# Optimization experiments

Measured on AMD Instinct MI355X. Metric: run time of the kernel, lower is better.

The kernel has to match this reference:

```python
import jax, jax.numpy as jnp
import numpy as np

K = 20
EPS = 1e-5


def knn_idx(x, k=K):
    # x: [B, C, N]; negative squared pairwise distance, take k largest (nearest)
    xt = jnp.swapaxes(x, 1, 2)  # [B, N, C]
    inner = -2.0 * jnp.einsum('bnc,bmc->bnm', xt, xt)
    xx = jnp.sum(x * x, axis=1)  # [B, N]
    dist = -xx[:, :, None] - inner - xx[:, None, :]  # [B, N, N] = -||xi-xj||^2
    _, idx = jax.lax.top_k(dist, k)  # [B, N, k]
    return idx


def edge_features(x, k=K):
    # returns [B, 2C, N, k] = concat(neighbor - center, center)
    idx = knn_idx(x, k)
    xt = jnp.swapaxes(x, 1, 2)  # [B, N, C]
    neigh = jax.vmap(lambda xb, ib: xb[ib])(xt, idx)  # [B, N, k, C]
    center = jnp.broadcast_to(xt[:, :, None, :], neigh.shape)
    feat = jnp.concatenate((neigh - center, center), axis=-1)  # [B, N, k, 2C]
    return jnp.transpose(feat, (0, 3, 1, 2))  # [B, 2C, N, k]


def bn_relu(y, g, b, axes):
    # batch-norm (training-mode batch stats, biased var) + ReLU; channel axis=1
    mu = jnp.mean(y, axis=axes, keepdims=True)
    var = jnp.mean(jnp.square(y - mu), axis=axes, keepdims=True)
    shape = [1] * y.ndim
    shape[1] = -1
    yhat = (y - mu) * jax.lax.rsqrt(var + EPS)
    return jax.nn.relu(yhat * g.reshape(shape) + b.reshape(shape))


def attn_pool(y):
    # softmax over neighbor axis, weighted sum: [B, C, N, k] -> [B, C, N]
    a = jax.nn.softmax(y, axis=-1)
    return jnp.sum(y * a, axis=-1)


def reference(x, W1, g1, b1, W2, g2, b2, W3, g3, b3):
    feat = edge_features(x)  # [B, 6, N, k]
    h1 = bn_relu(jnp.einsum('oc,bcnk->bonk', W1, feat), g1, b1, (0, 2, 3))  # [B,64,N,k]
    x1 = attn_pool(h1)  # [B, 64, N]
    h2 = bn_relu(jnp.einsum('oc,bcnk->bonk', W2, h1), g2, b2, (0, 2, 3))  # [B,128,N,k]
    x2 = attn_pool(h2)  # [B, 128, N]
    cat = jnp.concatenate((x1, x2), axis=1)  # [B, 192, N]
    out = bn_relu(jnp.einsum('oc,bcn->bon', W3, cat), g3, b3, (0, 2))  # [B,256,N]
    return out


def setup_inputs() -> dict:
    key = jax.random.key(0)
    ks = jax.random.split(key, 4)
    B, C, N = 8, 3, 4096
    return {
        'x': jax.random.normal(ks[0], (B, C, N), jnp.float32),
        'W1': jax.random.normal(ks[1], (64, 6), jnp.float32) * 0.1,
        'g1': jnp.ones((64,), jnp.float32),
        'b1': jnp.zeros((64,), jnp.float32),
        'W2': jax.random.normal(ks[2], (128, 64), jnp.float32) * 0.1,
        'g2': jnp.ones((128,), jnp.float32),
        'b2': jnp.zeros((128,), jnp.float32),
        'W3': jax.random.normal(ks[3], (256, 192), jnp.float32) * 0.1,
        'g3': jnp.ones((256,), jnp.float32),
        'b3': jnp.zeros((256,), jnp.float32),
    }
```

## Files before the change

kernel.cpp:

```cpp
#include <hip/hip_runtime.h>

namespace {
constexpr int Bn  = 8;
constexpr int Nn  = 4096;
constexpr int KKn = 20;
constexpr int C1n = 64;
constexpr int C2n = 128;
constexpr int C3n = 256;
constexpr float EPSc = 1e-5f;
constexpr float INV_CNT1 = 1.0f / (8.0f * 4096.0f * 20.0f);
constexpr float INV_CNT3 = 1.0f / (8.0f * 4096.0f);
constexpr float INFK = 3.0e38f;
constexpr size_t IDX_N = (size_t)Bn * Nn * KKn;
constexpr int NBLK_KNN = (Bn * Nn) / 16;
}

#define DEVI __device__ __forceinline__

__global__ void k_zero(float* __restrict__ p) {
    const int i = blockIdx.x * 256 + threadIdx.x;
    if (i < 33664) p[i] = 0.0f;
}

DEVI void ins3(float d, int j, float& m0, float& m1, float& m2,
               int& j0, int& j1, int& j2) {
    if (d < m2) {
        if (d < m1) {
            m2 = m1; j2 = j1;
            if (d < m0) { m1 = m0; j1 = j0; m0 = d; j0 = j; }
            else        { m1 = d;  j1 = j; }
        } else { m2 = d; j2 = j; }
    }
}

__global__ __launch_bounds__(256) void k_knn(const float* __restrict__ x,
                                             int* __restrict__ idxout,
                                             float* __restrict__ Pbuf) {
    __shared__ int   lidx[16][KKn];
    __shared__ float red[4][27];
    const int b = blockIdx.y;
    const float* xb = x + (size_t)b * 3 * Nn;
    const int lane = threadIdx.x & 63;
    const int wave = threadIdx.x >> 6;
    const int rowbase = blockIdx.x * 16 + wave * 4;

    for (int su = 0; su < 2; ++su) {
        const int rA = rowbase + su * 2;
        const int rB = rA + 1;
        const float pxA = xb[rA], pyA = xb[Nn + rA], pzA = xb[2 * Nn + rA];
        const float pxB = xb[rB], pyB = xb[Nn + rB], pzB = xb[2 * Nn + rB];
        float mA0 = INFK, mA1 = INFK, mA2 = INFK;
        float mB0 = INFK, mB1 = INFK, mB2 = INFK;
        int jA0 = -1, jA1 = -1, jA2 = -1;
        int jB0 = -1, jB1 = -1, jB2 = -1;
        #pragma unroll 8
        for (int t = 0; t < 64; ++t) {
            const int j = t * 64 + lane;
            const float xj = xb[j], yj = xb[Nn + j], zj = xb[2 * Nn + j];
            const float dxA = pxA - xj, dyA = pyA - yj, dzA = pzA - zj;
            const float dA = fmaf(dxA, dxA, fmaf(dyA, dyA, dzA * dzA));
            const float dxB = pxB - xj, dyB = pyB - yj, dzB = pzB - zj;
            const float dB = fmaf(dxB, dxB, fmaf(dyB, dyB, dzB * dzB));
            ins3(dA, j, mA0, mA1, mA2, jA0, jA1, jA2);
            ins3(dB, j, mB0, mB1, mB2, jB0, jB1, jB2);
        }
        int nvA = 3, nvB = 3;
        for (int s = 0; s < KKn; ++s) {
            float bdA = (nvA > 0) ? mA0 : INFK;
            int   bjA = (nvA > 0) ? jA0 : -1;
            float bdB = (nvB > 0) ? mB0 : INFK;
            int   bjB = (nvB > 0) ? jB0 : -1;
            #pragma unroll
            for (int off = 32; off; off >>= 1) {
                const float odA = __shfl_xor(bdA, off);
                const int   ojA = __shfl_xor(bjA, off);
                const float odB = __shfl_xor(bdB, off);
                const int   ojB = __shfl_xor(bjB, off);
                if (odA < bdA || (odA == bdA && (unsigned)ojA < (unsigned)bjA)) { bdA = odA; bjA = ojA; }
                if (odB < bdB || (odB == bdB && (unsigned)ojB < (unsigned)bjB)) { bdB = odB; bjB = ojB; }
            }
            if (lane == 0) {
                lidx[wave * 4 + su * 2][s]     = bjA;
                lidx[wave * 4 + su * 2 + 1][s] = bjB;
            }
            if (nvA > 0 && jA0 == bjA) {
                mA0 = mA1; jA0 = jA1; mA1 = mA2; jA1 = jA2; --nvA;
                if (nvA == 0 && s < KKn - 1) {
                    mA0 = mA1 = mA2 = INFK; jA0 = jA1 = jA2 = -1;
                    #pragma unroll 1
                    for (int t = 0; t < 64; ++t) {
                        const int j = t * 64 + lane;
                        const float dx = pxA - xb[j], dy = pyA - xb[Nn + j], dz = pzA - xb[2 * Nn + j];
                        const float d = fmaf(dx, dx, fmaf(dy, dy, dz * dz));
                        if ((d > bdA) || (d == bdA && j > bjA))
                            ins3(d, j, mA0, mA1, mA2, jA0, jA1, jA2);
                    }
                    nvA = 3;
                }
            }
            if (nvB > 0 && jB0 == bjB) {
                mB0 = mB1; jB0 = jB1; mB1 = mB2; jB1 = jB2; --nvB;
                if (nvB == 0 && s < KKn - 1) {
                    mB0 = mB1 = mB2 = INFK; jB0 = jB1 = jB2 = -1;
                    #pragma unroll 1
                    for (int t = 0; t < 64; ++t) {
                        const int j = t * 64 + lane;
                        const float dx = pxB - xb[j], dy = pyB - xb[Nn + j], dz = pzB - xb[2 * Nn + j];
                        const float d = fmaf(dx, dx, fmaf(dy, dy, dz * dz));
                        if ((d > bdB) || (d == bdB && j > bjB))
                            ins3(d, j, mB0, mB1, mB2, jB0, jB1, jB2);
                    }
                    nvB = 3;
                }
            }
        }
    }
    __syncthreads();

    float S[6] = {};
    float M[21] = {};
    #pragma unroll
    for (int rep = 0; rep < 2; ++rep) {
        const int w = rep * 64 + lane;
        if (w < 4 * KKn) {
            const int r  = (w * 3277) >> 16;
            const int kk = w - r * 20;
            const int rowg = rowbase + r;
            const int j = lidx[wave * 4 + r][kk];
            const float cx = xb[rowg], cy = xb[Nn + rowg], cz = xb[2 * Nn + rowg];
            const float e[6] = { xb[j] - cx, xb[Nn + j] - cy, xb[2 * Nn + j] - cz, cx, cy, cz };
            int q = 0;
            #pragma unroll
            for (int a = 0; a < 6; ++a) {
                S[a] += e[a];
                #pragma unroll
                for (int bb = a; bb < 6; ++bb) { M[q] = fmaf(e[a], e[bb], M[q]); ++q; }
            }
            idxout[(size_t)(b * Nn + rowbase) * KKn + w] = j;
        }
    }
    #pragma unroll
    for (int i = 0; i < 6; ++i) {
        float t = S[i];
        #pragma unroll
        for (int off = 1; off < 64; off <<= 1) t += __shfl_xor(t, off);
        S[i] = t;
    }
    #pragma unroll
    for (int i = 0; i < 21; ++i) {
        float t = M[i];
        #pragma unroll
        for (int off = 1; off < 64; off <<= 1) t += __shfl_xor(t, off);
        M[i] = t;
    }
    if (lane == 0) {
        #pragma unroll
        for (int i = 0; i < 6; ++i) red[wave][i] = S[i];
        #pragma unroll
        for (int i = 0; i < 21; ++i) red[wave][6 + i] = M[i];
    }
    __syncthreads();
    if (threadIdx.x < 27) {
        const int i = threadIdx.x;
        const int blk = blockIdx.y * gridDim.x + blockIdx.x;
        Pbuf[blk * 32 + i] = red[0][i] + red[1][i] + red[2][i] + red[3][i];
    }
}

__global__ __launch_bounds__(256) void k_statK(const float* __restrict__ Pbuf,
                                               float* __restrict__ statK) {
    __shared__ float red[8][27];
    const int tid = threadIdx.x;
    const int i  = tid & 31;
    const int c0 = tid >> 5;
    if (i < 27) {
        float s = 0.f;
        for (int c = c0; c < NBLK_KNN; c += 8) s += Pbuf[c * 32 + i];
        red[c0][i] = s;
    }
    __syncthreads();
    if (tid < 27) {
        float s = 0.f;
        #pragma unroll
        for (int c = 0; c < 8; ++c) s += red[c][tid];
        statK[tid] = s;
    }
}

DEVI void bn1_coef(const float* __restrict__ statK, const float* __restrict__ W1,
                   const float* __restrict__ g1, const float* __restrict__ b1,
                   int o, float& a1, float& be1, float* w1r) {
    #pragma unroll
    for (int c = 0; c < 6; ++c) w1r[c] = W1[o * 6 + c];
    float s1 = 0.f, q1 = 0.f;
    #pragma unroll
    for (int a = 0; a < 6; ++a) s1 = fmaf(w1r[a], statK[a], s1);
    int qi = 6;
    #pragma unroll
    for (int a = 0; a < 6; ++a) {
        #pragma unroll
        for (int bb = a; bb < 6; ++bb) {
            const float coef = (a == bb ? 1.f : 2.f) * w1r[a] * w1r[bb];
            q1 = fmaf(coef, statK[qi], q1); ++qi;
        }
    }
    const float mu  = s1 * INV_CNT1;
    const float var = q1 * INV_CNT1 - mu * mu;
    const float rs  = rsqrtf(var + EPSc);
    a1  = rs * g1[o];
    be1 = fmaf(-mu, a1, b1[o]);
}

template <bool POOL>
DEVI void conv1_phase1(const float* __restrict__ x, const int* __restrict__ idx,
                       float a1, float be1, const float* w1r,
                       float* __restrict__ cat, int b, int n0, int tid,
                       float (*hhat)[64], float* sAcc) {
    const int o = tid & 63;
    const int wave = tid >> 6;
    const float* xb = x + (size_t)b * 3 * Nn;
    #pragma unroll
    for (int pp = 0; pp < 2; ++pp) {
        const int p = wave * 2 + pp;
        const int n = n0 + p;
        const float cx = xb[n], cy = xb[Nn + n], cz = xb[2 * Nn + n];
        const float t2 = fmaf(w1r[3], cx, fmaf(w1r[4], cy, w1r[5] * cz));
        float hk[KKn];
        #pragma unroll
        for (int kk = 0; kk < KKn; ++kk) {
            const int j = idx[(size_t)(b * Nn + n) * KKn + kk];
            const float dx = xb[j] - cx, dy = xb[Nn + j] - cy, dz = xb[2 * Nn + j] - cz;
            float h = fmaf(w1r[0], dx, fmaf(w1r[1], dy, fmaf(w1r[2], dz, t2)));
            h = fmaxf(fmaf(h, a1, be1), 0.0f);
            hk[kk] = h;
            hhat[p * KKn + kk][o] = h;
            if (POOL) *sAcc += h;
        }
        if (POOL) {
            float mx = hk[0];
            #pragma unroll
            for (int kk = 1; kk < KKn; ++kk) mx = fmaxf(mx, hk[kk]);
            float se = 0.0f, sw = 0.0f;
            #pragma unroll
            for (int kk = 0; kk < KKn; ++kk) {
                const float e = __expf(hk[kk] - mx);
                se += e;
                sw = fmaf(hk[kk], e, sw);
            }
            cat[(size_t)(b * Nn + n) * 192 + o] = sw / se;
        }
    }
}

__global__ __launch_bounds__(256) void k_conv1(const float* __restrict__ x,
        const int* __restrict__ idx,
        const float* __restrict__ W1, const float* __restrict__ g1, const float* __restrict__ b1,
        const float* __restrict__ statK,
        float* __restrict__ Mbuf, float* __restrict__ S64,
        float* __restrict__ cat) {
    __shared__ float hhat[160][64];
    __shared__ float redS[4][64];
    const int tid = threadIdx.x;
    const int b  = blockIdx.x >> 7;
    const int n0 = (blockIdx.x & 127) * 32;
    float a1, be1, w1r[6];
    bn1_coef(statK, W1, g1, b1, tid & 63, a1, be1, w1r);
    const int abase = (tid >> 4) * 4;
    const int bbase = (tid & 15) * 4;
    float acc[4][4] = {};
    float sAcc = 0.f;
    for (int pass = 0; pass < 4; ++pass) {
        if (pass) __syncthreads();
        conv1_phase1<true>(x, idx, a1, be1, w1r, cat, b, n0 + pass * 8, tid, hhat, &sAcc);
        __syncthreads();
        #pragma unroll 2
        for (int p = 0; p < 160; ++p) {
            const float4 hav = *reinterpret_cast<const float4*>(&hhat[p][abase]);
            const float4 hbv = *reinterpret_cast<const float4*>(&hhat[p][bbase]);
            const float ha_[4] = { hav.x, hav.y, hav.z, hav.w };
            const float hb_[4] = { hbv.x, hbv.y, hbv.z, hbv.w };
            #pragma unroll
            for (int i = 0; i < 4; ++i)
                #pragma unroll
                for (int jj = 0; jj < 4; ++jj)
                    acc[i][jj] = fmaf(ha_[i], hb_[jj], acc[i][jj]);
        }
    }
    float* Mb = Mbuf + ((blockIdx.x & 7) << 12);
    #pragma unroll
    for (int i = 0; i < 4; ++i)
        #pragma unroll
        for (int jj = 0; jj < 4; ++jj)
            atomicAdd(&Mb[(abase + i) * 64 + bbase + jj], acc[i][jj]);
    redS[tid >> 6][tid & 63] = sAcc;
    __syncthreads();
    if (tid < 64)
        atomicAdd(&S64[tid], redS[0][tid] + redS[1][tid] + redS[2][tid] + redS[3][tid]);
}

__global__ __launch_bounds__(256) void k_stats2(const float* __restrict__ Mbuf,
        const float* __restrict__ S64, const float* __restrict__ W2,
        const float* __restrict__ g2, const float* __restrict__ b2,
        float* __restrict__ AB2) {
    __shared__ float ms[4096];
    __shared__ float w2s[16][64];
    const int tid = threadIdx.x;
    for (int e = tid; e < 4096; e += 256) {
        float t = 0.f;
        #pragma unroll
        for (int r = 0; r < 8; ++r) t += Mbuf[r * 4096 + e];
        ms[e] = t;
    }
    const int c0 = blockIdx.x * 16;
    for (int t = tid; t < 16 * 64; t += 256)
        w2s[t >> 6][t & 63] = W2[(c0 + (t >> 6)) * 64 + (t & 63)];
    __syncthreads();
    const int cl = tid >> 4;
    const int gl = tid & 15;
    const int c  = c0 + cl;
    float q2 = 0.f, s2 = 0.f;
    #pragma unroll
    for (int ai = 0; ai < 4; ++ai) {
        const int a = gl * 4 + ai;
        float inner = 0.f;
        for (int bq = 0; bq < 64; ++bq) {
            const int bb = (bq + 4 * gl) & 63;
            inner = fmaf(w2s[cl][bb], ms[a * 64 + bb], inner);
        }
        q2 = fmaf(w2s[cl][a], inner, q2);
        s2 = fmaf(w2s[cl][a], S64[a], s2);
    }
    #pragma unroll
    for (int off = 1; off < 16; off <<= 1) {
        q2 += __shfl_xor(q2, off);
        s2 += __shfl_xor(s2, off);
    }
    if (gl == 0) {
        const float mu  = s2 * INV_CNT1;
        const float var = q2 * INV_CNT1 - mu * mu;
        const float rs  = rsqrtf(var + EPSc);
        const float a2  = rs * g2[c];
        AB2[c]         = a2;
        AB2[C2n + c]   = fmaf(-mu, a2, b2[c]);
    }
}

__global__ __launch_bounds__(256) void k_conv2(const float* __restrict__ x,
        const int* __restrict__ idx,
        const float* __restrict__ W1, const float* __restrict__ g1, const float* __restrict__ b1,
        const float* __restrict__ W2, const float* __restrict__ AB2,
        const float* __restrict__ statK,
        float* __restrict__ cat) {
    __shared__ float hhat[160][64];
    __shared__ float w2s[C2n][68];
    const int tid = threadIdx.x;
    const int b   = blockIdx.x >> 8;
    const int nb  = (blockIdx.x & 255) * 16;
    float a1, be1, w1r[6];
    bn1_coef(statK, W1, g1, b1, tid & 63, a1, be1, w1r);
    for (int t = tid; t < C2n * C1n; t += 256) w2s[t >> 6][t & 63] = W2[t];

    const int q = tid & 31;
    const int p = tid >> 5;
    float a2[4], be2[4];
    #pragma unroll
    for (int m = 0; m < 4; ++m) {
        const int ch = q + 32 * m;
        a2[m]  = AB2[ch];
        be2[m] = AB2[C2n + ch];
    }

    for (int g = 0; g < 2; ++g) {
        const int n0 = nb + g * 8;
        if (g) __syncthreads();
        conv1_phase1<false>(x, idx, a1, be1, w1r, cat, b, n0, tid, hhat, nullptr);
        __syncthreads();

        const int n = n0 + p;
        float acc[4][KKn] = {};
        for (int oc = 0; oc < 16; ++oc) {
            float4 w[4];
            #pragma unroll
            for (int m = 0; m < 4; ++m)
                w[m] = *reinterpret_cast<const float4*>(&w2s[q + 32 * m][oc * 4]);
            #pragma unroll
            for (int kk = 0; kk < KKn; ++kk) {
                const float4 h = *reinterpret_cast<const float4*>(&hhat[p * KKn + kk][oc * 4]);
                #pragma unroll
                for (int m = 0; m < 4; ++m) {
                    acc[m][kk] = fmaf(w[m].x, h.x, acc[m][kk]);
                    acc[m][kk] = fmaf(w[m].y, h.y, acc[m][kk]);
                    acc[m][kk] = fmaf(w[m].z, h.z, acc[m][kk]);
                    acc[m][kk] = fmaf(w[m].w, h.w, acc[m][kk]);
                }
            }
        }
        #pragma unroll
        for (int m = 0; m < 4; ++m) {
            float v[KKn];
            float mx = 0.0f;
            #pragma unroll
            for (int kk = 0; kk < KKn; ++kk) {
                v[kk] = fmaxf(fmaf(acc[m][kk], a2[m], be2[m]), 0.0f);
                mx = fmaxf(mx, v[kk]);
            }
            float se = 0.0f, sw = 0.0f;
            #pragma unroll
            for (int kk = 0; kk < KKn; ++kk) {
                const float e = __expf(v[kk] - mx);
                se += e;
                sw = fmaf(v[kk], e, sw);
            }
            cat[(size_t)(b * Nn + n) * 192 + 64 + q + 32 * m] = sw / se;
        }
    }
}

__global__ __launch_bounds__(256) void k_fc(const float* __restrict__ cat,
        const float* __restrict__ W3,
        float* __restrict__ stats3, float* __restrict__ out) {
    __shared__ float w3s[C3n][52];
    __shared__ float ctf[32 * 192];
    const int tid = threadIdx.x;
    const int b  = blockIdx.x >> 7;
    const int n0 = (blockIdx.x & 127) * 32;
    const size_t base = (size_t)(b * Nn + n0) * 192;
    for (int t = tid; t < 32 * 192; t += 256) ctf[t] = cat[base + t];
    const int o3a = tid & 127;
    const int ph  = tid >> 7;
    float acc[2][16] = {};
    for (int ch = 0; ch < 4; ++ch) {
        __syncthreads();
        for (int t = tid; t < 256 * 48; t += 256) {
            const int row = t / 48, col = t - row * 48;
            w3s[row][col] = W3[row * 192 + ch * 48 + col];
        }
        __syncthreads();
        for (int c4 = 0; c4 < 12; ++c4) {
            const int c = c4 * 4;
            const float4 wA = *reinterpret_cast<const float4*>(&w3s[o3a][c]);
            const float4 wB = *reinterpret_cast<const float4*>(&w3s[o3a + 128][c]);
            #pragma unroll
            for (int p = 0; p < 16; ++p) {
                const int gp = ph * 16 + p;
                const float4 h = *reinterpret_cast<const float4*>(&ctf[gp * 192 + ch * 48 + c]);
                acc[0][p] = fmaf(wA.x, h.x, acc[0][p]);
                acc[0][p] = fmaf(wA.y, h.y, acc[0][p]);
                acc[0][p] = fmaf(wA.z, h.z, acc[0][p]);
                acc[0][p] = fmaf(wA.w, h.w, acc[0][p]);
                acc[1][p] = fmaf(wB.x, h.x, acc[1][p]);
                acc[1][p] = fmaf(wB.y, h.y, acc[1][p]);
                acc[1][p] = fmaf(wB.z, h.z, acc[1][p]);
                acc[1][p] = fmaf(wB.w, h.w, acc[1][p]);
            }
        }
    }
    #pragma unroll
    for (int half = 0; half < 2; ++half) {
        const int o3 = o3a + half * 128;
        float s = 0.0f, qq = 0.0f;
        #pragma unroll
        for (int p = 0; p < 16; ++p) {
            const float v = acc[half][p];
            s += v;
            qq = fmaf(v, v, qq);
            out[(size_t)(b * C3n + o3) * Nn + n0 + ph * 16 + p] = v;
        }
        atomicAdd(&stats3[o3], s);
        atomicAdd(&stats3[C3n + o3], qq);
    }
}

__global__ __launch_bounds__(256) void k_bnout(const float* __restrict__ stats3,
        const float* __restrict__ g3, const float* __restrict__ b3,
        float* __restrict__ out) {
    __shared__ float al[C3n], be[C3n];
    const int tid = threadIdx.x;
    {
        const int ch = tid;
        const float mu  = stats3[ch] * INV_CNT3;
        const float var = stats3[C3n + ch] * INV_CNT3 - mu * mu;
        const float rs  = rsqrtf(var + EPSc);
        al[ch] = rs * g3[ch];
        be[ch] = fmaf(-mu, al[ch], b3[ch]);
    }
    __syncthreads();
    const int total = Bn * C3n * Nn / 4;
    float4* o4 = reinterpret_cast<float4*>(out);
    for (int i = blockIdx.x * 256 + tid; i < total; i += gridDim.x * 256) {
        const int ch = (i >> 10) & 255;
        float4 v = o4[i];
        const float a = al[ch], bb = be[ch];
        v.x = fmaxf(fmaf(v.x, a, bb), 0.0f);
        v.y = fmaxf(fmaf(v.y, a, bb), 0.0f);
        v.z = fmaxf(fmaf(v.z, a, bb), 0.0f);
        v.w = fmaxf(fmaf(v.w, a, bb), 0.0f);
        o4[i] = v;
    }
}

extern "C" void kernel_launch(void* const* d_in, const int* in_sizes, int n_in,
                              void* d_out, int out_size, void* d_ws, size_t ws_size,
                              hipStream_t stream) {
    const float* x  = (const float*)d_in[0];
    const float* W1 = (const float*)d_in[1];
    const float* g1 = (const float*)d_in[2];
    const float* b1 = (const float*)d_in[3];
    const float* W2 = (const float*)d_in[4];
    const float* g2 = (const float*)d_in[5];
    const float* b2 = (const float*)d_in[6];
    const float* W3 = (const float*)d_in[7];
    const float* g3 = (const float*)d_in[8];
    const float* b3 = (const float*)d_in[9];
    float* out = (float*)d_out;

    int*   idx   = (int*)d_ws;
    float* fws   = (float*)d_ws;
    float* statK = fws + IDX_N;
    float* Mbuf  = statK + 64;
    float* S64   = Mbuf + 32768;
    float* AB2   = S64 + 64;
    float* st3   = AB2 + 256;
    float* cat   = st3 + 512;
    float* Pbuf  = cat;

    k_zero<<<132, 256, 0, stream>>>(statK);
    k_knn<<<dim3(Nn / 16, Bn), 256, 0, stream>>>(x, idx, Pbuf);
    k_statK<<<1, 256, 0, stream>>>(Pbuf, statK);
    k_conv1<<<Bn * Nn / 32, 256, 0, stream>>>(x, idx, W1, g1, b1, statK, Mbuf, S64, cat);
    k_stats2<<<8, 256, 0, stream>>>(Mbuf, S64, W2, g2, b2, AB2);
    k_conv2<<<Bn * Nn / 16, 256, 0, stream>>>(x, idx, W1, g1, b1, W2, AB2, statK, cat);
    k_fc<<<Bn * Nn / 32, 256, 0, stream>>>(cat, W3, st3, out);
    k_bnout<<<2048, 256, 0, stream>>>(st3, g3, b3, out);
}
```

Measured before the change: 1.222 ms.

## Keep per-lane top-5 in KNN and fall back to exact recompute rarely

Each lane now keeps its 5 nearest candidates instead of 3 during the main distance scan. The 20-step wave merge then runs without rescans. Only if some lane's candidates run out does the wave redo the row with the old exact top-k routine. This removes the frequent in-loop rescans of all 4096 points that the 3-deep lists caused. In exchange it adds register pressure (launch bounds raised to request 4 blocks per CU) and makes the main insertion slightly more expensive.

```diff
diff --git a/kernel.cpp b/kernel.cpp
--- a/kernel.cpp
+++ b/kernel.cpp
@@ -33,9 +33,68 @@
     }
 }
 
-__global__ __launch_bounds__(256) void k_knn(const float* __restrict__ x,
-                                             int* __restrict__ idxout,
-                                             float* __restrict__ Pbuf) {
+DEVI void ins5(float d, int j, float& m0, float& m1, float& m2, float& m3, float& m4,
+               int& j0, int& j1, int& j2, int& j3, int& j4) {
+    if (d < m4) {
+        if (d < m3) {
+            m4 = m3; j4 = j3;
+            if (d < m2) {
+                m3 = m2; j3 = j2;
+                if (d < m1) {
+                    m2 = m1; j2 = j1;
+                    if (d < m0) { m1 = m0; j1 = j0; m0 = d; j0 = j; }
+                    else        { m1 = d;  j1 = j; }
+                } else { m2 = d; j2 = j; }
+            } else { m3 = d; j3 = j; }
+        } else { m4 = d; j4 = j; }
+    }
+}
+
+DEVI void row_topk_exact(const float* __restrict__ xb, int row, int lane,
+                         int* __restrict__ lrow) {
+    const float px = xb[row], py = xb[Nn + row], pz = xb[2 * Nn + row];
+    float m0 = INFK, m1 = INFK, m2 = INFK;
+    int   j0 = -1, j1 = -1, j2 = -1;
+    #pragma unroll 1
+    for (int t = 0; t < 64; ++t) {
+        const int j = t * 64 + lane;
+        const float dx = px - xb[j], dy = py - xb[Nn + j], dz = pz - xb[2 * Nn + j];
+        const float d = fmaf(dx, dx, fmaf(dy, dy, dz * dz));
+        ins3(d, j, m0, m1, m2, j0, j1, j2);
+    }
+    int nv = 3;
+    #pragma unroll 1
+    for (int s = 0; s < KKn; ++s) {
+        float bd = (nv > 0) ? m0 : INFK;
+        int   bj = (nv > 0) ? j0 : -1;
+        #pragma unroll
+        for (int off = 32; off; off >>= 1) {
+            const float od = __shfl_xor(bd, off);
+            const int   oj = __shfl_xor(bj, off);
+            if (od < bd || (od == bd && (unsigned)oj < (unsigned)bj)) { bd = od; bj = oj; }
+        }
+        if (lane == 0) lrow[s] = bj;
+        if (nv > 0 && j0 == bj) {
+            m0 = m1; j0 = j1; m1 = m2; j1 = j2; --nv;
+            if (nv == 0 && s < KKn - 1) {
+                m0 = m1 = m2 = INFK; j0 = j1 = j2 = -1;
+                #pragma unroll 1
+                for (int t = 0; t < 64; ++t) {
+                    const int j = t * 64 + lane;
+                    const float dx = px - xb[j], dy = py - xb[Nn + j], dz = pz - xb[2 * Nn + j];
+                    const float d = fmaf(dx, dx, fmaf(dy, dy, dz * dz));
+                    if ((d > bd) || (d == bd && j > bj))
+                        ins3(d, j, m0, m1, m2, j0, j1, j2);
+                }
+                nv = 3;
+            }
+        }
+    }
+}
+
+__global__ __launch_bounds__(256, 4) void k_knn(const float* __restrict__ x,
+                                                int* __restrict__ idxout,
+                                                float* __restrict__ Pbuf) {
     __shared__ int   lidx[16][KKn];
     __shared__ float red[4][27];
     const int b = blockIdx.y;
@@ -49,11 +108,11 @@
         const int rB = rA + 1;
         const float pxA = xb[rA], pyA = xb[Nn + rA], pzA = xb[2 * Nn + rA];
         const float pxB = xb[rB], pyB = xb[Nn + rB], pzB = xb[2 * Nn + rB];
-        float mA0 = INFK, mA1 = INFK, mA2 = INFK;
-        float mB0 = INFK, mB1 = INFK, mB2 = INFK;
-        int jA0 = -1, jA1 = -1, jA2 = -1;
-        int jB0 = -1, jB1 = -1, jB2 = -1;
-        #pragma unroll 8
+        float mA0 = INFK, mA1 = INFK, mA2 = INFK, mA3 = INFK, mA4 = INFK;
+        float mB0 = INFK, mB1 = INFK, mB2 = INFK, mB3 = INFK, mB4 = INFK;
+        int jA0 = -1, jA1 = -1, jA2 = -1, jA3 = -1, jA4 = -1;
+        int jB0 = -1, jB1 = -1, jB2 = -1, jB3 = -1, jB4 = -1;
+        #pragma unroll 4
         for (int t = 0; t < 64; ++t) {
             const int j = t * 64 + lane;
             const float xj = xb[j], yj = xb[Nn + j], zj = xb[2 * Nn + j];
@@ -61,10 +120,11 @@
             const float dA = fmaf(dxA, dxA, fmaf(dyA, dyA, dzA * dzA));
             const float dxB = pxB - xj, dyB = pyB - yj, dzB = pzB - zj;
             const float dB = fmaf(dxB, dxB, fmaf(dyB, dyB, dzB * dzB));
-            ins3(dA, j, mA0, mA1, mA2, jA0, jA1, jA2);
-            ins3(dB, j, mB0, mB1, mB2, jB0, jB1, jB2);
-        }
-        int nvA = 3, nvB = 3;
+            ins5(dA, j, mA0, mA1, mA2, mA3, mA4, jA0, jA1, jA2, jA3, jA4);
+            ins5(dB, j, mB0, mB1, mB2, mB3, mB4, jB0, jB1, jB2, jB3, jB4);
+        }
+        int nvA = 5, nvB = 5;
+        bool badA = false, badB = false;
         for (int s = 0; s < KKn; ++s) {
             float bdA = (nvA > 0) ? mA0 : INFK;
             int   bjA = (nvA > 0) ? jA0 : -1;
@@ -84,36 +144,18 @@
                 lidx[wave * 4 + su * 2 + 1][s] = bjB;
             }
             if (nvA > 0 && jA0 == bjA) {
-                mA0 = mA1; jA0 = jA1; mA1 = mA2; jA1 = jA2; --nvA;
-                if (nvA == 0 && s < KKn - 1) {
-                    mA0 = mA1 = mA2 = INFK; jA0 = jA1 = jA2 = -1;
-                    #pragma unroll 1
-                    for (int t = 0; t < 64; ++t) {
-                        const int j = t * 64 + lane;
-                        const float dx = pxA - xb[j], dy = pyA - xb[Nn + j], dz = pzA - xb[2 * Nn + j];
-                        const float d = fmaf(dx, dx, fmaf(dy, dy, dz * dz));
-                        if ((d > bdA) || (d == bdA && j > bjA))
-                            ins3(d, j, mA0, mA1, mA2, jA0, jA1, jA2);
-                    }
-                    nvA = 3;
-                }
+                mA0 = mA1; jA0 = jA1; mA1 = mA2; jA1 = jA2;
+                mA2 = mA3; jA2 = jA3; mA3 = mA4; jA3 = jA4; --nvA;
+                if (nvA == 0 && s < KKn - 1) badA = true;
             }
             if (nvB > 0 && jB0 == bjB) {
-                mB0 = mB1; jB0 = jB1; mB1 = mB2; jB1 = jB2; --nvB;
-                if (nvB == 0 && s < KKn - 1) {
-                    mB0 = mB1 = mB2 = INFK; jB0 = jB1 = jB2 = -1;
-                    #pragma unroll 1
-                    for (int t = 0; t < 64; ++t) {
-                        const int j = t * 64 + lane;
-                        const float dx = pxB - xb[j], dy = pyB - xb[Nn + j], dz = pzB - xb[2 * Nn + j];
-                        const float d = fmaf(dx, dx, fmaf(dy, dy, dz * dz));
-                        if ((d > bdB) || (d == bdB && j > bjB))
-                            ins3(d, j, mB0, mB1, mB2, jB0, jB1, jB2);
-                    }
-                    nvB = 3;
-                }
-            }
-        }
+                mB0 = mB1; jB0 = jB1; mB1 = mB2; jB1 = jB2;
+                mB2 = mB3; jB2 = jB3; mB3 = mB4; jB3 = jB4; --nvB;
+                if (nvB == 0 && s < KKn - 1) badB = true;
+            }
+        }
+        if (__any(badA)) row_topk_exact(xb, rA, lane, &lidx[wave * 4 + su * 2][0]);
+        if (__any(badB)) row_topk_exact(xb, rB, lane, &lidx[wave * 4 + su * 2 + 1][0]);
     }
     __syncthreads();
 
```

New measurement: 2.012 ms. 64.7% more time.
